# Optimization experiments

Hardware: AMD Instinct MI355X
Metric: run time of the kernel (lower is better)

Reference implementation:

```python
import jax, jax.numpy as jnp
import numpy as np

NUM_STEPS = 151            # num_steps from __init__
STEP = 2.0 / (NUM_STEPS - 1)
HALF = (NUM_STEPS - 1) // 2  # bin offset: t_j = -1 + j*STEP, 1/STEP = HALF
N = 4096
D = 512
NUM_CLASSES = 751


def _soft_histogram(s, mask, size):
    # Triangular-kernel (linear) soft binning, equivalent to the original
    # indsa/indsb masked-repeat construction: each similarity s in
    # [t_{j-1}, t_j] contributes (1-frac) to bin j-1 and frac to bin j.
    x = s / STEP
    k = jnp.floor(x)           # zero-gradient, plays the role of s_repeat_floor
    frac = x - k               # (s - (t_j - STEP)) / STEP
    kI = k.astype(jnp.int32)
    idx_lo = jnp.clip(kI + HALF, 0, NUM_STEPS - 1)
    idx_hi = jnp.clip(kI + HALF + 1, 0, NUM_STEPS - 1)
    hist = jnp.zeros((NUM_STEPS,), dtype=s.dtype)
    hist = hist.at[idx_lo].add((1.0 - frac) * mask)
    hist = hist.at[idx_hi].add(frac * mask)
    return hist / size


def setup_inputs() -> dict:
    key = jax.random.key(0)
    kf, kc = jax.random.split(key)
    return {
        "features": jax.random.normal(kf, (N, D), dtype=jnp.float32),
        "classes": jax.random.randint(kc, (N,), 0, NUM_CLASSES, dtype=jnp.int32),
    }


def reference(features, classes):
    # L2Normalization
    f = features / jnp.linalg.norm(features, axis=1, keepdims=True)
    dists = f @ f.T                                   # [N, N] cosine sims
    iu, ju = np.triu_indices(features.shape[0], 1)    # static upper-tri pairs
    s = dists[iu, ju]                                 # [P] P = N(N-1)/2
    pos = (classes[iu] == classes[ju]).astype(s.dtype)
    neg = 1.0 - pos
    hist_pos = _soft_histogram(s, pos, jnp.sum(pos))
    hist_neg = _soft_histogram(s, neg, jnp.sum(neg))
    cdf_pos = jnp.cumsum(hist_pos)                    # tril-masked column sums == cumsum
    return jnp.sum(hist_neg * cdf_pos)
```

## Files before the change

### kernel.cpp

```cpp
#include <hip/hip_runtime.h>
#include <math.h>

#define N 4096
#define D 512
#define NUM_STEPS 151
#define HALF_BINS 75
#define INV_STEP 75.0f
#define NUM_CLASSES 751
#define P_TOTAL 8386560.0f

#define WS_SUM_ALL 0
#define WS_POS_CNT 1
#define WS_SUM_POS 2
#define WS_S_POS   3
#define WS_G_OFF   8
#define WS_LIST_OFF 1024
#define MAXP (1 << 18)
#define WS_FEAT_OFF (WS_LIST_OFF + MAXP)
#define WS_FEATB_OFF (WS_FEAT_OFF + N * D)
#define WS_IDX_OFF  (WS_FEATB_OFF + N * D / 2)
#define WS_OFFS_OFF (WS_IDX_OFF + N)
#define WS_POFF_OFF (WS_OFFS_OFF + NUM_CLASSES + 1)

typedef __bf16 bf16x8 __attribute__((ext_vector_type(8)));
typedef float floatx4 __attribute__((ext_vector_type(4)));

__global__ __launch_bounds__(256) void k_normalize(const float* __restrict__ feat,
                                                   float* __restrict__ nf,
                                                   __bf16* __restrict__ nfb) {
    int row = blockIdx.x;
    int t = threadIdx.x;
    const float* fr = feat + (size_t)row * D;
    float a = fr[t];
    float b = fr[t + 256];
    float ss = a * a + b * b;
    for (int o = 32; o > 0; o >>= 1) ss += __shfl_down(ss, o, 64);
    __shared__ float wsum[4];
    int lane = t & 63, wid = t >> 6;
    if (lane == 0) wsum[wid] = ss;
    __syncthreads();
    float tot = wsum[0] + wsum[1] + wsum[2] + wsum[3];
    float inv = 1.0f / sqrtf(tot);
    float na = a * inv, nb = b * inv;
    nf[(size_t)row * D + t] = na;
    nf[(size_t)row * D + t + 256] = nb;
    nfb[(size_t)row * D + t] = (__bf16)na;
    nfb[(size_t)row * D + t + 256] = (__bf16)nb;
}

__global__ __launch_bounds__(256) void k_sort(const int* __restrict__ cls,
                                              int* __restrict__ rowIdx,
                                              int* __restrict__ offs,
                                              int* __restrict__ pairOffs,
                                              int* __restrict__ posCntOut) {
    __shared__ int hcnt[NUM_CLASSES];
    __shared__ int hoff[NUM_CLASSES];
    __shared__ int poff[NUM_CLASSES];
    __shared__ int wsumR[4], wsumP[4];
    int t = threadIdx.x;
    for (int c = t; c < NUM_CLASSES; c += 256) hcnt[c] = 0;
    __syncthreads();
    for (int n = t; n < N; n += 256) atomicAdd(&hcnt[cls[n]], 1);
    __syncthreads();

    int c0 = t * 3;
    int cntPreR[3], cntPreP[3];
    int myR = 0, myP = 0;
    #pragma unroll
    for (int k = 0; k < 3; ++k) {
        int c = c0 + k;
        int cnt = (c < NUM_CLASSES) ? hcnt[c] : 0;
        cntPreR[k] = myR; cntPreP[k] = myP;
        myR += cnt;
        myP += cnt * (cnt - 1) / 2;
    }
    int lane = t & 63, wv = t >> 6;
    int incR = myR, incP = myP;
    for (int o = 1; o < 64; o <<= 1) {
        int rr = __shfl_up(incR, o, 64);
        int pp = __shfl_up(incP, o, 64);
        if (lane >= o) { incR += rr; incP += pp; }
    }
    if (lane == 63) { wsumR[wv] = incR; wsumP[wv] = incP; }
    __syncthreads();
    int baseR = 0, baseP = 0;
    for (int w = 0; w < wv; ++w) { baseR += wsumR[w]; baseP += wsumP[w]; }
    int exR = baseR + incR - myR;
    int exP = baseP + incP - myP;
    #pragma unroll
    for (int k = 0; k < 3; ++k) {
        int c = c0 + k;
        if (c < NUM_CLASSES) { hoff[c] = exR + cntPreR[k]; poff[c] = exP + cntPreP[k]; }
    }
    __syncthreads();

    for (int c = t; c < NUM_CLASSES; c += 256) hcnt[c] = hoff[c];
    __syncthreads();
    for (int n = t; n < N; n += 256) {
        int p = atomicAdd(&hcnt[cls[n]], 1);
        rowIdx[p] = n;
    }
    for (int c = t; c < NUM_CLASSES; c += 256) { offs[c] = hoff[c]; pairOffs[c] = poff[c]; }
    if (t == 0) {
        int totR = wsumR[0] + wsumR[1] + wsumR[2] + wsumR[3];
        int totP = wsumP[0] + wsumP[1] + wsumP[2] + wsumP[3];
        offs[NUM_CLASSES] = totR;
        pairOffs[NUM_CLASSES] = totP;
        *posCntOut = totP;
    }
}

__global__ __launch_bounds__(256) void k_pospairs3(const float* __restrict__ nf,
                                                   const int* __restrict__ rowIdx,
                                                   const int* __restrict__ offs,
                                                   const int* __restrict__ pairOffs,
                                                   float* __restrict__ posS) {
    int c = blockIdx.x;
    int o0 = offs[c], o1 = offs[c + 1];
    int nc = o1 - o0;
    if (nc < 2) return;
    int nPairs = nc * (nc - 1) / 2;
    int pBase = pairOffs[c];
    int lane = threadIdx.x & 63;
    int wave = threadIdx.x >> 6;
    for (int p = wave; p < nPairs; p += 4) {
        int a = 0, rem = p;
        while (rem >= nc - 1 - a) { rem -= nc - 1 - a; ++a; }
        int b = a + 1 + rem;
        int ri = rowIdx[o0 + a], rj = rowIdx[o0 + b];
        const float4* x4 = (const float4*)(nf + (size_t)ri * D);
        const float4* y4 = (const float4*)(nf + (size_t)rj * D);
        float4 xa = x4[lane * 2], xb = x4[lane * 2 + 1];
        float4 ya = y4[lane * 2], yb = y4[lane * 2 + 1];
        float s = xa.x * ya.x + xa.y * ya.y + xa.z * ya.z + xa.w * ya.w
                + xb.x * yb.x + xb.y * yb.y + xb.z * yb.z + xb.w * yb.w;
        for (int o = 32; o > 0; o >>= 1) s += __shfl_down(s, o, 64);
        if (lane == 0) posS[pBase + p] = s;
    }
}

__global__ __launch_bounds__(256) void k_build_cdf(const float* __restrict__ posS,
                                                   const int* __restrict__ posCnt,
                                                   float* __restrict__ G,
                                                   float* __restrict__ sumPosOut,
                                                   float* __restrict__ sPosOut) {
    __shared__ float hist[NUM_STEPS];
    __shared__ float Gs[NUM_STEPS];
    int t = threadIdx.x;
    int C = *posCnt;
    if (C > MAXP) C = MAXP;
    for (int b = t; b < NUM_STEPS; b += 256) hist[b] = 0.f;
    __syncthreads();
    for (int p = t; p < C; p += 256) {
        float s = posS[p];
        float x = s * INV_STEP;
        float kf = floorf(x);
        float frac = x - kf;
        int kI = (int)kf;
        int lo = min(max(kI + HALF_BINS, 0), NUM_STEPS - 1);
        int hi = min(max(kI + HALF_BINS + 1, 0), NUM_STEPS - 1);
        atomicAdd(&hist[lo], 1.0f - frac);
        atomicAdd(&hist[hi], frac);
    }
    __syncthreads();
    if (t == 0) {
        float invC = (C > 0) ? (1.0f / (float)C) : 0.f;
        float acc = 0.f;
        for (int b = 0; b < NUM_STEPS; ++b) {
            acc += hist[b];
            Gs[b] = acc * invC;
        }
    }
    __syncthreads();
    for (int b = t; b < NUM_STEPS; b += 256) G[b] = Gs[b];
    float ps = 0.f;
    for (int p = t; p < C; p += 256) {
        float s = posS[p];
        float x = s * INV_STEP;
        float kf = floorf(x);
        float frac = x - kf;
        int kI = (int)kf;
        int lo = min(max(kI + HALF_BINS, 0), NUM_STEPS - 1);
        int hi = min(max(kI + HALF_BINS + 1, 0), NUM_STEPS - 1);
        ps += (1.f - frac) * Gs[lo] + frac * Gs[hi];
    }
    for (int o = 32; o > 0; o >>= 1) ps += __shfl_down(ps, o, 64);
    __shared__ float wsum[4];
    int lane = t & 63, wid = t >> 6;
    if (lane == 0) wsum[wid] = ps;
    __syncthreads();
    if (t == 0) {
        *sumPosOut = wsum[0] + wsum[1] + wsum[2] + wsum[3];
        *sPosOut = (float)C;
    }
}

#define TILES_1D 32
#define LDSS 40

__global__ __launch_bounds__(256) void k_gram(const __bf16* __restrict__ nfb,
                                              const float* __restrict__ G,
                                              float* __restrict__ sumAll) {
    int bid = blockIdx.x;
    int ti = 0, rem = bid;
    while (rem >= TILES_1D - ti) { rem -= TILES_1D - ti; ++ti; }
    int tj = ti + rem;

    __shared__ __align__(16) __bf16 As[128 * LDSS];
    __shared__ __align__(16) __bf16 Bs[128 * LDSS];
    __shared__ float Gs[NUM_STEPS];

    int tid = threadIdx.x;
    for (int b = tid; b < NUM_STEPS; b += 256) Gs[b] = G[b];

    int lane = tid & 63;
    int wave = tid >> 6;
    int wm = (wave >> 1) * 64;
    int wn = (wave & 1) * 64;
    int fr = lane & 15;
    int fk = (lane >> 4) * 8;

    int rowA0 = ti * 128, rowB0 = tj * 128;

    floatx4 acc[4][4] = {};

    int e0 = tid * 8;
    int e1 = e0 + 2048;
    int r0 = e0 >> 5, c0 = e0 & 31;
    int r1 = e1 >> 5, c1 = e1 & 31;

    for (int kb = 0; kb < D / 32; ++kb) {
        int kbase = kb * 32;
        *(float4*)(&As[r0 * LDSS + c0]) = *(const float4*)(nfb + (size_t)(rowA0 + r0) * D + kbase + c0);
        *(float4*)(&As[r1 * LDSS + c1]) = *(const float4*)(nfb + (size_t)(rowA0 + r1) * D + kbase + c1);
        *(float4*)(&Bs[r0 * LDSS + c0]) = *(const float4*)(nfb + (size_t)(rowB0 + r0) * D + kbase + c0);
        *(float4*)(&Bs[r1 * LDSS + c1]) = *(const float4*)(nfb + (size_t)(rowB0 + r1) * D + kbase + c1);
        __syncthreads();

        bf16x8 a[4], b[4];
        #pragma unroll
        for (int r = 0; r < 4; ++r)
            a[r] = *(const bf16x8*)(&As[(wm + r * 16 + fr) * LDSS + fk]);
        #pragma unroll
        for (int c = 0; c < 4; ++c)
            b[c] = *(const bf16x8*)(&Bs[(wn + c * 16 + fr) * LDSS + fk]);

        #pragma unroll
        for (int r = 0; r < 4; ++r)
            #pragma unroll
            for (int c = 0; c < 4; ++c)
                acc[r][c] = __builtin_amdgcn_mfma_f32_16x16x32_bf16(a[r], b[c], acc[r][c], 0, 0, 0);
        __syncthreads();
    }

    int crow = (lane >> 4) * 4;
    int ccol = lane & 15;
    float gsum = 0.f;
    #pragma unroll
    for (int r = 0; r < 4; ++r) {
        #pragma unroll
        for (int c = 0; c < 4; ++c) {
            #pragma unroll
            for (int reg = 0; reg < 4; ++reg) {
                int gi = rowA0 + wm + r * 16 + crow + reg;
                int gj = rowB0 + wn + c * 16 + ccol;
                if (gi < gj) {
                    float s = acc[r][c][reg];
                    float x = s * INV_STEP;
                    float kf = floorf(x);
                    float frac = x - kf;
                    int kI = (int)kf;
                    int lo = min(max(kI + HALF_BINS, 0), NUM_STEPS - 1);
                    int hi = min(max(kI + HALF_BINS + 1, 0), NUM_STEPS - 1);
                    gsum += (1.f - frac) * Gs[lo] + frac * Gs[hi];
                }
            }
        }
    }
    for (int o = 32; o > 0; o >>= 1) gsum += __shfl_down(gsum, o, 64);
    __shared__ float wsum[4];
    if ((tid & 63) == 0) wsum[tid >> 6] = gsum;
    __syncthreads();
    if (tid == 0) atomicAdd(sumAll, wsum[0] + wsum[1] + wsum[2] + wsum[3]);
}

__global__ void k_final(const float* __restrict__ wsf, float* __restrict__ out) {
    float C = wsf[WS_S_POS];
    float sneg = P_TOTAL - C;
    out[0] = (wsf[WS_SUM_ALL] - wsf[WS_SUM_POS]) / sneg;
}

extern "C" void kernel_launch(void* const* d_in, const int* in_sizes, int n_in,
                              void* d_out, int out_size, void* d_ws, size_t ws_size,
                              hipStream_t stream) {
    const float* feat = (const float*)d_in[0];
    const int* cls = (const int*)d_in[1];
    float* out = (float*)d_out;
    float* wsf = (float*)d_ws;
    int* wsi = (int*)d_ws;

    hipMemsetAsync(d_ws, 0, 4096, stream);

    float* nf = wsf + WS_FEAT_OFF;
    __bf16* nfb = (__bf16*)(wsf + WS_FEATB_OFF);
    float* posS = wsf + WS_LIST_OFF;
    float* G = wsf + WS_G_OFF;
    int* rowIdx = wsi + WS_IDX_OFF;
    int* offs = wsi + WS_OFFS_OFF;
    int* pairOffs = wsi + WS_POFF_OFF;

    k_normalize<<<N, 256, 0, stream>>>(feat, nf, nfb);
    k_sort<<<1, 256, 0, stream>>>(cls, rowIdx, offs, pairOffs, wsi + WS_POS_CNT);
    k_pospairs3<<<NUM_CLASSES, 256, 0, stream>>>(nf, rowIdx, offs, pairOffs, posS);
    k_build_cdf<<<1, 256, 0, stream>>>(posS, wsi + WS_POS_CNT, G,
                                       wsf + WS_SUM_POS, wsf + WS_S_POS);
    int nTiles = TILES_1D * (TILES_1D + 1) / 2;
    k_gram<<<nTiles, 256, 0, stream>>>(nfb, G, wsf + WS_SUM_ALL);
    k_final<<<1, 1, 0, stream>>>(wsf, out);
}
```

Measured before the change: 158.5 us.

## Fuse pipeline into three launches using last-block-done atomics and drop memset

Merges normalize and class sort into one grid, with an extra block doing the sort and zeroing the workspace counters. Folds the CDF build into the positive-pair kernel through a last-block-done atomic counter, and folds the final division into the gram kernel the same way. This removes the memset and three kernel launches along with their launch gaps. In exchange it adds threadfence and atomic serialization, and it relies on the sort block's zeroing being visible before later kernels run.

```diff
diff --git a/kernel.cpp b/kernel.cpp
--- a/kernel.cpp
+++ b/kernel.cpp
@@ -13,6 +13,8 @@
 #define WS_POS_CNT 1
 #define WS_SUM_POS 2
 #define WS_S_POS   3
+#define WS_DONE2   4
+#define WS_DONE3   5
 #define WS_G_OFF   8
 #define WS_LIST_OFF 1024
 #define MAXP (1 << 18)
@@ -25,39 +27,47 @@
 typedef __bf16 bf16x8 __attribute__((ext_vector_type(8)));
 typedef float floatx4 __attribute__((ext_vector_type(4)));
 
-__global__ __launch_bounds__(256) void k_normalize(const float* __restrict__ feat,
+__global__ __launch_bounds__(256) void k_norm_sort(const float* __restrict__ feat,
+                                                   const int* __restrict__ cls,
                                                    float* __restrict__ nf,
-                                                   __bf16* __restrict__ nfb) {
-    int row = blockIdx.x;
+                                                   __bf16* __restrict__ nfb,
+                                                   int* __restrict__ rowIdx,
+                                                   int* __restrict__ offs,
+                                                   int* __restrict__ pairOffs,
+                                                   float* __restrict__ wsf,
+                                                   int* __restrict__ wsi) {
     int t = threadIdx.x;
-    const float* fr = feat + (size_t)row * D;
-    float a = fr[t];
-    float b = fr[t + 256];
-    float ss = a * a + b * b;
-    for (int o = 32; o > 0; o >>= 1) ss += __shfl_down(ss, o, 64);
-    __shared__ float wsum[4];
-    int lane = t & 63, wid = t >> 6;
-    if (lane == 0) wsum[wid] = ss;
-    __syncthreads();
-    float tot = wsum[0] + wsum[1] + wsum[2] + wsum[3];
-    float inv = 1.0f / sqrtf(tot);
-    float na = a * inv, nb = b * inv;
-    nf[(size_t)row * D + t] = na;
-    nf[(size_t)row * D + t + 256] = nb;
-    nfb[(size_t)row * D + t] = (__bf16)na;
-    nfb[(size_t)row * D + t + 256] = (__bf16)nb;
-}
-
-__global__ __launch_bounds__(256) void k_sort(const int* __restrict__ cls,
-                                              int* __restrict__ rowIdx,
-                                              int* __restrict__ offs,
-                                              int* __restrict__ pairOffs,
-                                              int* __restrict__ posCntOut) {
+    if (blockIdx.x < N) {
+        int row = blockIdx.x;
+        const float* fr = feat + (size_t)row * D;
+        float a = fr[t];
+        float b = fr[t + 256];
+        float ss = a * a + b * b;
+        for (int o = 32; o > 0; o >>= 1) ss += __shfl_down(ss, o, 64);
+        __shared__ float wsum[4];
+        int lane = t & 63, wid = t >> 6;
+        if (lane == 0) wsum[wid] = ss;
+        __syncthreads();
+        float tot = wsum[0] + wsum[1] + wsum[2] + wsum[3];
+        float inv = 1.0f / sqrtf(tot);
+        float na = a * inv, nb = b * inv;
+        nf[(size_t)row * D + t] = na;
+        nf[(size_t)row * D + t + 256] = nb;
+        nfb[(size_t)row * D + t] = (__bf16)na;
+        nfb[(size_t)row * D + t + 256] = (__bf16)nb;
+        return;
+    }
+
+    if (t == 0) {
+        wsf[WS_SUM_ALL] = 0.f;
+        wsf[WS_SUM_POS] = 0.f;
+        wsi[WS_DONE2] = 0;
+        wsi[WS_DONE3] = 0;
+    }
     __shared__ int hcnt[NUM_CLASSES];
     __shared__ int hoff[NUM_CLASSES];
     __shared__ int poff[NUM_CLASSES];
     __shared__ int wsumR[4], wsumP[4];
-    int t = threadIdx.x;
     for (int c = t; c < NUM_CLASSES; c += 256) hcnt[c] = 0;
     __syncthreads();
     for (int n = t; n < N; n += 256) atomicAdd(&hcnt[cls[n]], 1);
@@ -106,48 +116,57 @@
         int totP = wsumP[0] + wsumP[1] + wsumP[2] + wsumP[3];
         offs[NUM_CLASSES] = totR;
         pairOffs[NUM_CLASSES] = totP;
-        *posCntOut = totP;
+        wsi[WS_POS_CNT] = totP;
     }
 }
 
-__global__ __launch_bounds__(256) void k_pospairs3(const float* __restrict__ nf,
-                                                   const int* __restrict__ rowIdx,
-                                                   const int* __restrict__ offs,
-                                                   const int* __restrict__ pairOffs,
-                                                   float* __restrict__ posS) {
+__global__ __launch_bounds__(256) void k_pos_cdf(const float* __restrict__ nf,
+                                                 const int* __restrict__ rowIdx,
+                                                 const int* __restrict__ offs,
+                                                 const int* __restrict__ pairOffs,
+                                                 float* __restrict__ posS,
+                                                 float* __restrict__ G,
+                                                 float* __restrict__ wsf,
+                                                 int* __restrict__ wsi) {
     int c = blockIdx.x;
     int o0 = offs[c], o1 = offs[c + 1];
     int nc = o1 - o0;
-    if (nc < 2) return;
-    int nPairs = nc * (nc - 1) / 2;
-    int pBase = pairOffs[c];
-    int lane = threadIdx.x & 63;
-    int wave = threadIdx.x >> 6;
-    for (int p = wave; p < nPairs; p += 4) {
-        int a = 0, rem = p;
-        while (rem >= nc - 1 - a) { rem -= nc - 1 - a; ++a; }
-        int b = a + 1 + rem;
-        int ri = rowIdx[o0 + a], rj = rowIdx[o0 + b];
-        const float4* x4 = (const float4*)(nf + (size_t)ri * D);
-        const float4* y4 = (const float4*)(nf + (size_t)rj * D);
-        float4 xa = x4[lane * 2], xb = x4[lane * 2 + 1];
-        float4 ya = y4[lane * 2], yb = y4[lane * 2 + 1];
-        float s = xa.x * ya.x + xa.y * ya.y + xa.z * ya.z + xa.w * ya.w
-                + xb.x * yb.x + xb.y * yb.y + xb.z * yb.z + xb.w * yb.w;
-        for (int o = 32; o > 0; o >>= 1) s += __shfl_down(s, o, 64);
-        if (lane == 0) posS[pBase + p] = s;
-    }
-}
-
-__global__ __launch_bounds__(256) void k_build_cdf(const float* __restrict__ posS,
-                                                   const int* __restrict__ posCnt,
-                                                   float* __restrict__ G,
-                                                   float* __restrict__ sumPosOut,
-                                                   float* __restrict__ sPosOut) {
+    int t = threadIdx.x;
+    int lane = t & 63;
+    int wave = t >> 6;
+    if (nc >= 2) {
+        int nPairs = nc * (nc - 1) / 2;
+        int pBase = pairOffs[c];
+        for (int p = wave; p < nPairs; p += 4) {
+            int a = 0, rem = p;
+            while (rem >= nc - 1 - a) { rem -= nc - 1 - a; ++a; }
+            int b = a + 1 + rem;
+            int ri = rowIdx[o0 + a], rj = rowIdx[o0 + b];
+            const float4* x4 = (const float4*)(nf + (size_t)ri * D);
+            const float4* y4 = (const float4*)(nf + (size_t)rj * D);
+            float4 xa = x4[lane * 2], xb = x4[lane * 2 + 1];
+            float4 ya = y4[lane * 2], yb = y4[lane * 2 + 1];
+            float s = xa.x * ya.x + xa.y * ya.y + xa.z * ya.z + xa.w * ya.w
+                    + xb.x * yb.x + xb.y * yb.y + xb.z * yb.z + xb.w * yb.w;
+            for (int o = 32; o > 0; o >>= 1) s += __shfl_down(s, o, 64);
+            if (lane == 0) posS[pBase + p] = s;
+        }
+    }
+
+    __shared__ bool sdone;
+    __syncthreads();
+    if (t == 0) {
+        __threadfence();
+        int v = atomicAdd(&wsi[WS_DONE2], 1);
+        sdone = (v == (int)gridDim.x - 1);
+    }
+    __syncthreads();
+    if (!sdone) return;
+    __threadfence();
+
     __shared__ float hist[NUM_STEPS];
     __shared__ float Gs[NUM_STEPS];
-    int t = threadIdx.x;
-    int C = *posCnt;
+    int C = wsi[WS_POS_CNT];
     if (C > MAXP) C = MAXP;
     for (int b = t; b < NUM_STEPS; b += 256) hist[b] = 0.f;
     __syncthreads();
@@ -186,21 +205,23 @@
     }
     for (int o = 32; o > 0; o >>= 1) ps += __shfl_down(ps, o, 64);
     __shared__ float wsum[4];
-    int lane = t & 63, wid = t >> 6;
-    if (lane == 0) wsum[wid] = ps;
-    __syncthreads();
-    if (t == 0) {
-        *sumPosOut = wsum[0] + wsum[1] + wsum[2] + wsum[3];
-        *sPosOut = (float)C;
+    int wid = t >> 6;
+    if ((t & 63) == 0) wsum[wid] = ps;
+    __syncthreads();
+    if (t == 0) {
+        wsf[WS_SUM_POS] = wsum[0] + wsum[1] + wsum[2] + wsum[3];
+        wsf[WS_S_POS] = (float)C;
     }
 }
 
 #define TILES_1D 32
 #define LDSS 40
 
-__global__ __launch_bounds__(256) void k_gram(const __bf16* __restrict__ nfb,
-                                              const float* __restrict__ G,
-                                              float* __restrict__ sumAll) {
+__global__ __launch_bounds__(256) void k_gram_final(const __bf16* __restrict__ nfb,
+                                                    const float* __restrict__ G,
+                                                    float* __restrict__ wsf,
+                                                    int* __restrict__ wsi,
+                                                    float* __restrict__ out) {
     int bid = blockIdx.x;
     int ti = 0, rem = bid;
     while (rem >= TILES_1D - ti) { rem -= TILES_1D - ti; ++ti; }
@@ -281,13 +302,22 @@
     __shared__ float wsum[4];
     if ((tid & 63) == 0) wsum[tid >> 6] = gsum;
     __syncthreads();
-    if (tid == 0) atomicAdd(sumAll, wsum[0] + wsum[1] + wsum[2] + wsum[3]);
-}
-
-__global__ void k_final(const float* __restrict__ wsf, float* __restrict__ out) {
-    float C = wsf[WS_S_POS];
-    float sneg = P_TOTAL - C;
-    out[0] = (wsf[WS_SUM_ALL] - wsf[WS_SUM_POS]) / sneg;
+    if (tid == 0) atomicAdd(&wsf[WS_SUM_ALL], wsum[0] + wsum[1] + wsum[2] + wsum[3]);
+
+    __shared__ bool sdone;
+    if (tid == 0) {
+        __threadfence();
+        int v = atomicAdd(&wsi[WS_DONE3], 1);
+        sdone = (v == (int)gridDim.x - 1);
+    }
+    __syncthreads();
+    if (sdone && tid == 0) {
+        __threadfence();
+        float sAll = atomicAdd(&wsf[WS_SUM_ALL], 0.0f);
+        float C = wsf[WS_S_POS];
+        float sneg = P_TOTAL - C;
+        out[0] = (sAll - wsf[WS_SUM_POS]) / sneg;
+    }
 }
 
 extern "C" void kernel_launch(void* const* d_in, const int* in_sizes, int n_in,
@@ -299,8 +329,6 @@
     float* wsf = (float*)d_ws;
     int* wsi = (int*)d_ws;
 
-    hipMemsetAsync(d_ws, 0, 4096, stream);
-
     float* nf = wsf + WS_FEAT_OFF;
     __bf16* nfb = (__bf16*)(wsf + WS_FEATB_OFF);
     float* posS = wsf + WS_LIST_OFF;
@@ -309,12 +337,8 @@
     int* offs = wsi + WS_OFFS_OFF;
     int* pairOffs = wsi + WS_POFF_OFF;
 
-    k_normalize<<<N, 256, 0, stream>>>(feat, nf, nfb);
-    k_sort<<<1, 256, 0, stream>>>(cls, rowIdx, offs, pairOffs, wsi + WS_POS_CNT);
-    k_pospairs3<<<NUM_CLASSES, 256, 0, stream>>>(nf, rowIdx, offs, pairOffs, posS);
-    k_build_cdf<<<1, 256, 0, stream>>>(posS, wsi + WS_POS_CNT, G,
-                                       wsf + WS_SUM_POS, wsf + WS_S_POS);
+    k_norm_sort<<<N + 1, 256, 0, stream>>>(feat, cls, nf, nfb, rowIdx, offs, pairOffs, wsf, wsi);
+    k_pos_cdf<<<NUM_CLASSES, 256, 0, stream>>>(nf, rowIdx, offs, pairOffs, posS, G, wsf, wsi);
     int nTiles = TILES_1D * (TILES_1D + 1) / 2;
-    k_gram<<<nTiles, 256, 0, stream>>>(nfb, G, wsf + WS_SUM_ALL);
-    k_final<<<1, 1, 0, stream>>>(wsf, out);
+    k_gram_final<<<nTiles, 256, 0, stream>>>(nfb, G, wsf, wsi, out);
 }
```

After: 175.1 us. 10.5% more time.
